# Performance work log

Measured on AMD Instinct MI355X. Metric: run time of the kernel, lower is better.

The kernel has to match this reference:

```python
import jax, jax.numpy as jnp
import numpy as np

ALPHA = 0.2      # LeakyReLU negative slope
NEG_INF = -9e15  # mask value from the original module
EPS = 1e-8


def setup_inputs() -> dict:
    key = jax.random.key(0)
    k1, k2, k3, k4 = jax.random.split(key, 4)
    B, N, F_in, F_out = 8, 2048, 128, 64
    h = jax.random.normal(k1, (B, N, F_in), dtype=jnp.float32)
    u = jax.random.uniform(k2, (B, N, N), dtype=jnp.float32)
    adj = jnp.where(u > 0.9, u, 0.0)
    adj = jnp.maximum(adj, jnp.eye(N, dtype=jnp.float32)[None])
    # Xavier-uniform with gain 1.414 as in the torch init
    gain = 1.414
    bW = gain * np.sqrt(6.0 / (F_in + F_out))
    W = jax.random.uniform(k3, (F_in, F_out), jnp.float32, -bW, bW)
    ba = gain * np.sqrt(6.0 / (2 * F_out + 1))
    a = jax.random.uniform(k4, (2 * F_out, 1), jnp.float32, -ba, ba)
    return {"h": h, "adj": adj, "W": W, "a": a}


def reference(h, adj, W, a):
    # h: [B,N,Fin], adj: [B,N,N], W: [Fin,Fout], a: [2*Fout,1]
    F_out = W.shape[1]
    Wh = jnp.einsum('bnf,fo->bno', h, W)                      # [B,N,Fout]
    # Split-projection equivalent of cat([Wh_i, Wh_j]) @ a:
    # e[b,i,j] = leaky(Wh[b,i]@a1 + Wh[b,j]@a2)
    a1 = a[:F_out, 0]
    a2 = a[F_out:, 0]
    e = jax.nn.leaky_relu(
        (Wh @ a1)[:, :, None] + (Wh @ a2)[:, None, :],        # [B,N,N]
        negative_slope=ALPHA,
    )
    att = jnp.where(adj > 0, e, NEG_INF)
    att = jax.nn.softmax(att, axis=2)
    att = att * adj
    att = att / (jnp.sum(att, axis=2, keepdims=True) + EPS)
    h_prime = jnp.einsum('bij,bjo->bio', att, Wh)             # [B,N,Fout]
    return jax.nn.elu(h_prime)                                # concat=True -> ELU
```

## Files before the change

### kernel.cpp

```cpp
#include <hip/hip_runtime.h>
#include <hip/hip_bf16.h>
#include <stdint.h>

#define LRELU_ALPHA 0.2f
#define L2E 1.44269504f

constexpr int BB = 8, NN = 2048, FIN = 128, FOUT = 64;
constexpr int GEMM_ROWS = 32;
constexpr int NBLK_G = BB * NN / GEMM_ROWS;

typedef __attribute__((ext_vector_type(8))) short short8;
typedef __attribute__((ext_vector_type(4))) float f32x4;

__device__ __forceinline__ ushort bf16rn(float f) {
    __hip_bfloat16 h = __float2bfloat16(f);
    return *reinterpret_cast<ushort*>(&h);
}

#define HS 132
__global__ __launch_bounds__(256) void k_gemm_hw(const float* __restrict__ h,
                                                 const float* __restrict__ W,
                                                 const float* __restrict__ a,
                                                 ushort* __restrict__ WhP,
                                                 float* __restrict__ s1,
                                                 float* __restrict__ s2,
                                                 float* __restrict__ pmax) {
    __shared__ float hs[GEMM_ROWS * HS];
    __shared__ __align__(16) ushort fragbuf[2048];
    __shared__ float smax[16];
    const int tid = threadIdx.x;
    const int base = blockIdx.x * GEMM_ROWS;

    #pragma unroll
    for (int rep = 0; rep < 4; ++rep) {
        int flat4 = rep * 256 + tid;
        int row = flat4 >> 5, k4 = flat4 & 31;
        float4 v = *reinterpret_cast<const float4*>(h + (size_t)(base + row) * FIN + k4 * 4);
        *reinterpret_cast<float4*>(&hs[row * HS + k4 * 4]) = v;
    }
    __syncthreads();

    const int tr = tid >> 4;
    const int tc = tid & 15;
    float acc[2][4] = {};
    #pragma unroll 4
    for (int k = 0; k < FIN; ++k) {
        float4 wv = *reinterpret_cast<const float4*>(W + (size_t)k * FOUT + tc * 4);
        #pragma unroll
        for (int r = 0; r < 2; ++r) {
            float hv = hs[(tr * 2 + r) * HS + k];
            acc[r][0] = fmaf(hv, wv.x, acc[r][0]);
            acc[r][1] = fmaf(hv, wv.y, acc[r][1]);
            acc[r][2] = fmaf(hv, wv.z, acc[r][2]);
            acc[r][3] = fmaf(hv, wv.w, acc[r][3]);
        }
    }

    #pragma unroll
    for (int r = 0; r < 2; ++r) {
        const int jloc = tr * 2 + r;
        const int e = jloc & 7, kgrp = jloc >> 3;
        #pragma unroll
        for (int c = 0; c < 4; ++c) {
            const int col = tc * 4 + c;
            fragbuf[((col >> 4) * 64 + kgrp * 16 + (col & 15)) * 8 + e] = bf16rn(acc[r][c]);
        }
    }

    float a1c[4], a2c[4];
    #pragma unroll
    for (int c = 0; c < 4; ++c) {
        a1c[c] = a[tc * 4 + c];
        a2c[c] = a[FOUT + tc * 4 + c];
    }
    float maxp2 = -3.4e38f;
    #pragma unroll
    for (int r = 0; r < 2; ++r) {
        float p1 = acc[r][0] * a1c[0] + acc[r][1] * a1c[1] + acc[r][2] * a1c[2] + acc[r][3] * a1c[3];
        float p2 = acc[r][0] * a2c[0] + acc[r][1] * a2c[1] + acc[r][2] * a2c[2] + acc[r][3] * a2c[3];
        #pragma unroll
        for (int off = 1; off < 16; off <<= 1) {
            p1 += __shfl_xor(p1, off);
            p2 += __shfl_xor(p2, off);
        }
        if (tc == 0) {
            s1[base + tr * 2 + r] = p1;
            s2[base + tr * 2 + r] = p2;
            maxp2 = fmaxf(maxp2, p2);
        }
    }
    if (tc == 0) smax[tr] = maxp2;
    __syncthreads();

    const size_t region = ((size_t)((base >> 11) * 64 + ((base & 2047) >> 5))) * 2048;
    *reinterpret_cast<uint4*>(WhP + region + tid * 8) =
        *reinterpret_cast<const uint4*>(fragbuf + tid * 8);

    if (tid == 0) {
        float mm = smax[0];
        #pragma unroll
        for (int i = 1; i < 16; ++i) mm = fmaxf(mm, smax[i]);
        pmax[blockIdx.x] = mm;
    }
}

__global__ __launch_bounds__(256, 4) void k_attn(const float* __restrict__ adj,
                                                 const ushort* __restrict__ WhP,
                                                 const float* __restrict__ s1,
                                                 const float* __restrict__ s2,
                                                 const float* __restrict__ pmax,
                                                 float* __restrict__ out) {
    __shared__ float lacc[4][16][68];
    __shared__ float lS[4][16];

    const int tid = threadIdx.x;
    const int l = tid & 63, w = tid >> 6;
    const int li = l & 15, lk = l >> 4;
    const int blk = blockIdx.x;
    const int b = blk >> 7;
    const int rowbase = blk * 16;
    const int row_i = rowbase + li;

    float m = -3.4e38f;
    #pragma unroll
    for (int t = 0; t < 8; ++t) m = fmaxf(m, pmax[l + 64 * t]);
    #pragma unroll
    for (int off = 32; off > 0; off >>= 1) m = fmaxf(m, __shfl_xor(m, off));

    const float s1i = s1[row_i];
    const float cp = s1i + m;
    const float c = fmaxf(cp, LRELU_ALPHA * cp);
    const float cL = c * L2E;

    const float* __restrict__ adjp = adj + (size_t)row_i * NN + w * 512 + lk * 8;
    const float* __restrict__ s2p  = s2 + (size_t)b * NN + w * 512 + lk * 8;
    const ushort* __restrict__ whp = WhP + (size_t)b * 131072 + (size_t)(w * 16) * 2048 + l * 8;

    f32x4 acc0 = {0.f, 0.f, 0.f, 0.f};
    f32x4 acc1 = {0.f, 0.f, 0.f, 0.f};
    f32x4 acc2 = {0.f, 0.f, 0.f, 0.f};
    f32x4 acc3 = {0.f, 0.f, 0.f, 0.f};
    f32x4 accS = {0.f, 0.f, 0.f, 0.f};
    short8 ones;
    #pragma unroll
    for (int e = 0; e < 8; ++e) ones[e] = (short)0x3F80;

    float4 a0 = *reinterpret_cast<const float4*>(adjp);
    float4 a1 = *reinterpret_cast<const float4*>(adjp + 4);
    short8 b0 = *reinterpret_cast<const short8*>(whp);
    short8 b1 = *reinterpret_cast<const short8*>(whp + 512);
    short8 b2 = *reinterpret_cast<const short8*>(whp + 1024);
    short8 b3 = *reinterpret_cast<const short8*>(whp + 1536);

    #pragma unroll
    for (int t = 0; t < 16; ++t) {
        float4 na0, na1;
        short8 nb0, nb1, nb2, nb3;
        if (t < 15) {
            na0 = *reinterpret_cast<const float4*>(adjp + (t + 1) * 32);
            na1 = *reinterpret_cast<const float4*>(adjp + (t + 1) * 32 + 4);
            const ushort* np = whp + (t + 1) * 2048;
            nb0 = *reinterpret_cast<const short8*>(np);
            nb1 = *reinterpret_cast<const short8*>(np + 512);
            nb2 = *reinterpret_cast<const short8*>(np + 1024);
            nb3 = *reinterpret_cast<const short8*>(np + 1536);
        }
        const float4 v0 = *reinterpret_cast<const float4*>(s2p + t * 32);
        const float4 v1 = *reinterpret_cast<const float4*>(s2p + t * 32 + 4);

        short8 af;
        {
            float ev, lr, ex;
#define DOE(idx, AV, SV)                                                      \
            ev = s1i + (SV);                                                  \
            lr = fmaxf(ev, LRELU_ALPHA * ev);                                 \
            ex = exp2f(fmaf(lr, L2E, -cL));                                   \
            af[idx] = (short)bf16rn((AV) * ex);
            DOE(0, a0.x, v0.x) DOE(1, a0.y, v0.y) DOE(2, a0.z, v0.z) DOE(3, a0.w, v0.w)
            DOE(4, a1.x, v1.x) DOE(5, a1.y, v1.y) DOE(6, a1.z, v1.z) DOE(7, a1.w, v1.w)
#undef DOE
        }
        acc0 = __builtin_amdgcn_mfma_f32_16x16x32_bf16(af, b0, acc0, 0, 0, 0);
        acc1 = __builtin_amdgcn_mfma_f32_16x16x32_bf16(af, b1, acc1, 0, 0, 0);
        acc2 = __builtin_amdgcn_mfma_f32_16x16x32_bf16(af, b2, acc2, 0, 0, 0);
        acc3 = __builtin_amdgcn_mfma_f32_16x16x32_bf16(af, b3, acc3, 0, 0, 0);
        accS = __builtin_amdgcn_mfma_f32_16x16x32_bf16(af, ones, accS, 0, 0, 0);

        if (t < 15) {
            a0 = na0; a1 = na1;
            b0 = nb0; b1 = nb1; b2 = nb2; b3 = nb3;
        }
    }

    if (li == 0) {
        #pragma unroll
        for (int r = 0; r < 4; ++r) lS[w][lk * 4 + r] = accS[r];
    }

    #pragma unroll
    for (int r = 0; r < 4; ++r) {
        lacc[w][lk * 4 + r][0 * 16 + li] = acc0[r];
        lacc[w][lk * 4 + r][1 * 16 + li] = acc1[r];
        lacc[w][lk * 4 + r][2 * 16 + li] = acc2[r];
        lacc[w][lk * 4 + r][3 * 16 + li] = acc3[r];
    }

    __syncthreads();

    #pragma unroll
    for (int q = 0; q < 4; ++q) {
        const int idx = q * 256 + tid;
        const int row = idx >> 6, col = idx & 63;
        float v = lacc[0][row][col] + lacc[1][row][col] + lacc[2][row][col] + lacc[3][row][col];
        float S = lS[0][row] + lS[1][row] + lS[2][row] + lS[3][row];
        float o = v / S;
        o = o > 0.f ? o : expm1f(o);
        out[(size_t)(rowbase + row) * FOUT + col] = o;
    }
}

extern "C" void kernel_launch(void* const* d_in, const int* in_sizes, int n_in,
                              void* d_out, int out_size, void* d_ws, size_t ws_size,
                              hipStream_t stream) {
    (void)in_sizes; (void)n_in; (void)out_size; (void)ws_size;
    const float* h   = (const float*)d_in[0];
    const float* adj = (const float*)d_in[1];
    const float* W   = (const float*)d_in[2];
    const float* a   = (const float*)d_in[3];
    float* out = (float*)d_out;

    ushort* WhP = (ushort*)d_ws;
    float* s1w  = (float*)(WhP + (size_t)BB * NN * FOUT);
    float* s2w  = s1w + (size_t)BB * NN;
    float* pmaxw = s2w + (size_t)BB * NN;

    k_gemm_hw<<<NBLK_G, 256, 0, stream>>>(h, W, a, WhP, s1w, s2w, pmaxw);
    k_attn<<<BB * NN / 16, 256, 0, stream>>>(adj, WhP, s1w, s2w, pmaxw, out);
}
```

Before: 54.62 us.

## Split attention K-loop across 8 waves and compute row sums in VALU

The attention kernel now launches 512 threads (8 waves) per 16-row block, and each wave covers 256 columns instead of 512, so the loop trip count halves and more loads are in flight. The fifth MFMA against a ones vector is removed; row sums are accumulated in scalar registers from the rounded bf16 weights and reduced with cross-lane shuffles. The loop now always prefetches, clamping the final prefetch index instead of branching, and is partially unrolled. The cost is more LDS for the per-wave partials, an 8-way cross-wave reduction, and extra VALU adds per element.

New measurement: 50.87 us. 6.9% less time.

```diff
diff --git a/kernel.cpp b/kernel.cpp
--- a/kernel.cpp
+++ b/kernel.cpp
@@ -104,14 +104,14 @@
     }
 }
 
-__global__ __launch_bounds__(256, 4) void k_attn(const float* __restrict__ adj,
+__global__ __launch_bounds__(512, 8) void k_attn(const float* __restrict__ adj,
                                                  const ushort* __restrict__ WhP,
                                                  const float* __restrict__ s1,
                                                  const float* __restrict__ s2,
                                                  const float* __restrict__ pmax,
                                                  float* __restrict__ out) {
-    __shared__ float lacc[4][16][68];
-    __shared__ float lS[4][16];
+    __shared__ float lacc[8][16][68];
+    __shared__ float lS[8][16];
 
     const int tid = threadIdx.x;
     const int l = tid & 63, w = tid >> 6;
@@ -129,21 +129,17 @@
 
     const float s1i = s1[row_i];
     const float cp = s1i + m;
-    const float c = fmaxf(cp, LRELU_ALPHA * cp);
-    const float cL = c * L2E;
-
-    const float* __restrict__ adjp = adj + (size_t)row_i * NN + w * 512 + lk * 8;
-    const float* __restrict__ s2p  = s2 + (size_t)b * NN + w * 512 + lk * 8;
-    const ushort* __restrict__ whp = WhP + (size_t)b * 131072 + (size_t)(w * 16) * 2048 + l * 8;
+    const float cL = fmaxf(cp, LRELU_ALPHA * cp) * L2E;
+
+    const float* __restrict__ adjp = adj + (size_t)row_i * NN + w * 256 + lk * 8;
+    const float* __restrict__ s2p  = s2 + (size_t)b * NN + w * 256 + lk * 8;
+    const ushort* __restrict__ whp = WhP + (size_t)b * 131072 + (size_t)(w * 8) * 2048 + l * 8;
 
     f32x4 acc0 = {0.f, 0.f, 0.f, 0.f};
     f32x4 acc1 = {0.f, 0.f, 0.f, 0.f};
     f32x4 acc2 = {0.f, 0.f, 0.f, 0.f};
     f32x4 acc3 = {0.f, 0.f, 0.f, 0.f};
-    f32x4 accS = {0.f, 0.f, 0.f, 0.f};
-    short8 ones;
-    #pragma unroll
-    for (int e = 0; e < 8; ++e) ones[e] = (short)0x3F80;
+    float Sp = 0.f;
 
     float4 a0 = *reinterpret_cast<const float4*>(adjp);
     float4 a1 = *reinterpret_cast<const float4*>(adjp + 4);
@@ -152,30 +148,32 @@
     short8 b2 = *reinterpret_cast<const short8*>(whp + 1024);
     short8 b3 = *reinterpret_cast<const short8*>(whp + 1536);
 
-    #pragma unroll
-    for (int t = 0; t < 16; ++t) {
-        float4 na0, na1;
-        short8 nb0, nb1, nb2, nb3;
-        if (t < 15) {
-            na0 = *reinterpret_cast<const float4*>(adjp + (t + 1) * 32);
-            na1 = *reinterpret_cast<const float4*>(adjp + (t + 1) * 32 + 4);
-            const ushort* np = whp + (t + 1) * 2048;
-            nb0 = *reinterpret_cast<const short8*>(np);
-            nb1 = *reinterpret_cast<const short8*>(np + 512);
-            nb2 = *reinterpret_cast<const short8*>(np + 1024);
-            nb3 = *reinterpret_cast<const short8*>(np + 1536);
-        }
+    #pragma unroll 2
+    for (int t = 0; t < 8; ++t) {
+        const int tn = (t < 7) ? t + 1 : 7;
+        float4 na0 = *reinterpret_cast<const float4*>(adjp + tn * 32);
+        float4 na1 = *reinterpret_cast<const float4*>(adjp + tn * 32 + 4);
+        const ushort* np = whp + tn * 2048;
+        short8 nb0 = *reinterpret_cast<const short8*>(np);
+        short8 nb1 = *reinterpret_cast<const short8*>(np + 512);
+        short8 nb2 = *reinterpret_cast<const short8*>(np + 1024);
+        short8 nb3 = *reinterpret_cast<const short8*>(np + 1536);
+
         const float4 v0 = *reinterpret_cast<const float4*>(s2p + t * 32);
         const float4 v1 = *reinterpret_cast<const float4*>(s2p + t * 32 + 4);
 
         short8 af;
         {
-            float ev, lr, ex;
+            float ev, lr, ex, wv;
+            ushort ub;
 #define DOE(idx, AV, SV)                                                      \
             ev = s1i + (SV);                                                  \
             lr = fmaxf(ev, LRELU_ALPHA * ev);                                 \
             ex = exp2f(fmaf(lr, L2E, -cL));                                   \
-            af[idx] = (short)bf16rn((AV) * ex);
+            wv = (AV) * ex;                                                   \
+            ub = bf16rn(wv);                                                  \
+            Sp += __uint_as_float((uint32_t)ub << 16);                        \
+            af[idx] = (short)ub;
             DOE(0, a0.x, v0.x) DOE(1, a0.y, v0.y) DOE(2, a0.z, v0.z) DOE(3, a0.w, v0.w)
             DOE(4, a1.x, v1.x) DOE(5, a1.y, v1.y) DOE(6, a1.z, v1.z) DOE(7, a1.w, v1.w)
 #undef DOE
@@ -184,18 +182,15 @@
         acc1 = __builtin_amdgcn_mfma_f32_16x16x32_bf16(af, b1, acc1, 0, 0, 0);
         acc2 = __builtin_amdgcn_mfma_f32_16x16x32_bf16(af, b2, acc2, 0, 0, 0);
         acc3 = __builtin_amdgcn_mfma_f32_16x16x32_bf16(af, b3, acc3, 0, 0, 0);
-        accS = __builtin_amdgcn_mfma_f32_16x16x32_bf16(af, ones, accS, 0, 0, 0);
-
-        if (t < 15) {
-            a0 = na0; a1 = na1;
-            b0 = nb0; b1 = nb1; b2 = nb2; b3 = nb3;
-        }
-    }
-
-    if (li == 0) {
-        #pragma unroll
-        for (int r = 0; r < 4; ++r) lS[w][lk * 4 + r] = accS[r];
-    }
+
+        a0 = na0; a1 = na1;
+        b0 = nb0; b1 = nb1; b2 = nb2; b3 = nb3;
+    }
+
+    float Sred = Sp;
+    Sred += __shfl_xor(Sred, 16);
+    Sred += __shfl_xor(Sred, 32);
+    if (l < 16) lS[w][li] = Sred;
 
     #pragma unroll
     for (int r = 0; r < 4; ++r) {
@@ -204,15 +199,18 @@
         lacc[w][lk * 4 + r][2 * 16 + li] = acc2[r];
         lacc[w][lk * 4 + r][3 * 16 + li] = acc3[r];
     }
-
     __syncthreads();
 
     #pragma unroll
-    for (int q = 0; q < 4; ++q) {
-        const int idx = q * 256 + tid;
+    for (int q = 0; q < 2; ++q) {
+        const int idx = q * 512 + tid;
         const int row = idx >> 6, col = idx & 63;
-        float v = lacc[0][row][col] + lacc[1][row][col] + lacc[2][row][col] + lacc[3][row][col];
-        float S = lS[0][row] + lS[1][row] + lS[2][row] + lS[3][row];
+        float v = 0.f, S = 0.f;
+        #pragma unroll
+        for (int ww = 0; ww < 8; ++ww) {
+            v += lacc[ww][row][col];
+            S += lS[ww][row];
+        }
         float o = v / S;
         o = o > 0.f ? o : expm1f(o);
         out[(size_t)(rowbase + row) * FOUT + col] = o;
@@ -235,5 +233,5 @@
     float* pmaxw = s2w + (size_t)BB * NN;
 
     k_gemm_hw<<<NBLK_G, 256, 0, stream>>>(h, W, a, WhP, s1w, s2w, pmaxw);
-    k_attn<<<BB * NN / 16, 256, 0, stream>>>(adj, WhP, s1w, s2w, pmaxw, out);
-}
+    k_attn<<<BB * NN / 16, 512, 0, stream>>>(adj, WhP, s1w, s2w, pmaxw, out);
+}
```
